# Optimization experiments

Hardware: AMD Instinct MI355X
Metric: run time of the kernel (lower is better)

## Reference

```python
import jax, jax.numpy as jnp
import numpy as np

BN_EPS = 1e-5

def lrelu(x):
    return jax.nn.leaky_relu(x, 0.2)

def bn(x, g, b):
    # BatchNorm1d in training mode: biased batch stats over batch dim
    m = x.mean(0)
    v = ((x - m) ** 2).mean(0)
    return g * (x - m) / jnp.sqrt(v + BN_EPS) + b

def setup_inputs() -> dict:
    key = jax.random.key(0)
    ks = jax.random.split(key, 12)
    B, NOISE, H, V = 128, 128, 512, 5000
    s = lambda *sh: 1.0 / np.sqrt(sh[-1])
    inp = {
        "z": jax.random.normal(ks[0], (B, NOISE), jnp.float32),
        "temperature": jnp.ones((1,), jnp.float32),
        "num_steps": 128,
        "W_z2h": jax.random.normal(ks[1], (H, NOISE), jnp.float32) * s(H, NOISE),
        "b_z2h": jnp.zeros((H,), jnp.float32),
        "g1": jnp.ones((H,), jnp.float32), "be1": jnp.zeros((H,), jnp.float32),
        "emb": jax.random.normal(ks[2], (V, H), jnp.float32),
        "g2": jnp.ones((2 * H,), jnp.float32), "be2": jnp.zeros((2 * H,), jnp.float32),
        "W_ih": jax.random.normal(ks[3], (3 * H, 2 * H), jnp.float32) * s(3 * H, 2 * H),
        "b_ih": jnp.zeros((3 * H,), jnp.float32),
        "W_hh": jax.random.normal(ks[4], (3 * H, H), jnp.float32) * s(3 * H, H),
        "b_hh": jnp.zeros((3 * H,), jnp.float32),
        "g3": jnp.ones((H,), jnp.float32), "be3": jnp.zeros((H,), jnp.float32),
        "W_h2o": jax.random.normal(ks[5], (V, H), jnp.float32) * s(V, H),
        "b_h2o": jnp.zeros((V,), jnp.float32),
    }
    return inp

def gru_cell(x, h, W_ih, b_ih, W_hh, b_hh):
    gi = x @ W_ih.T + b_ih
    gh = h @ W_hh.T + b_hh
    ir, iz, inn = jnp.split(gi, 3, axis=1)
    hr, hz, hn = jnp.split(gh, 3, axis=1)
    r = jax.nn.sigmoid(ir + hr)
    zt = jax.nn.sigmoid(iz + hz)
    n = jnp.tanh(inn + r * hn)
    return (1.0 - zt) * n + zt * h

def reference(z, temperature, W_z2h, b_z2h, g1, be1, emb, g2, be2,
              W_ih, b_ih, W_hh, b_hh, g3, be3, W_h2o, b_h2o, num_steps):
    V = W_h2o.shape[0]
    SOS = V - 1
    zbn = bn(lrelu(z @ W_z2h.T + b_z2h), g1, be1)  # [B,H]
    h0 = zbn
    prev0 = jnp.full((z.shape[0],), SOS, dtype=jnp.int32)
    key0 = jax.random.key(42)

    def step(carry, _):
        h, prev, key = carry
        key, sub = jax.random.split(key)
        x = lrelu(emb[prev])                                    # [B,H]
        si = bn(jnp.concatenate([x, zbn], axis=1), g2, be2)     # [B,2H]
        h = gru_cell(si, h, W_ih, b_ih, W_hh, b_hh)
        o = bn(lrelu(h), g3, be3)
        logits = o @ W_h2o.T + b_h2o                            # [B,V]
        u = jax.random.uniform(sub, logits.shape, jnp.float32, 1e-20, 1.0)
        gum = -jnp.log(-jnp.log(u))
        out = jax.nn.softmax((logits + gum) / temperature, axis=-1)
        prev = jnp.argmax(out, axis=-1).astype(jnp.int32)
        return (h, prev, key), out

    _, outs = jax.lax.scan(step, (h0, prev0, key0), None, length=num_steps)
    return jnp.transpose(outs, (1, 0, 2))  # [B, num_steps, V]
```

## Files before the change

### kernel.cpp

```cpp
#include <hip/hip_runtime.h>
#include <cstdint>
#include <cstddef>

#define B_SZ 128
#define NOISE_SZ 128
#define H 512
#define V_SZ 5000
#define BN_EPS 1e-5f

#define S1D 1099511627776.0
#define S2D 68719476736.0

#define SCRA_OFF 0
#define H_OFF    65536
#define GH_OFF   131072
#define GIZ_OFF  327680
#define SH_OFF   524288
#define SCRB_OFF 528896
#define AMX_OFF  594432

__device__ __forceinline__ uint32_t rotl32(uint32_t v, int r) {
  return (v << r) | (v >> (32 - r));
}

__device__ __forceinline__ void threefry2x32(uint32_t k0, uint32_t k1,
                                             uint32_t x0, uint32_t x1,
                                             uint32_t& o0, uint32_t& o1) {
  uint32_t k2 = k0 ^ k1 ^ 0x1BD11BDAu;
  x0 += k0; x1 += k1;
#define TFR(r) { x0 += x1; x1 = rotl32(x1, (r)); x1 ^= x0; }
  TFR(13) TFR(15) TFR(26) TFR(6)
  x0 += k1; x1 += k2 + 1u;
  TFR(17) TFR(29) TFR(16) TFR(24)
  x0 += k2; x1 += k0 + 2u;
  TFR(13) TFR(15) TFR(26) TFR(6)
  x0 += k0; x1 += k1 + 3u;
  TFR(17) TFR(29) TFR(16) TFR(24)
  x0 += k1; x1 += k2 + 4u;
  TFR(13) TFR(15) TFR(26) TFR(6)
  x0 += k2; x1 += k0 + 5u;
#undef TFR
  o0 = x0; o1 = x1;
}

struct U2 { uint32_t a, b; };
constexpr U2 tf_c(uint32_t k0, uint32_t k1, uint32_t x0, uint32_t x1) {
  uint32_t k2 = k0 ^ k1 ^ 0x1BD11BDAu;
  x0 += k0; x1 += k1;
#define TFRC(r) { x0 += x1; x1 = (uint32_t)((x1 << (r)) | (x1 >> (32 - (r)))); x1 ^= x0; }
  TFRC(13) TFRC(15) TFRC(26) TFRC(6)
  x0 += k1; x1 += k2 + 1u;
  TFRC(17) TFRC(29) TFRC(16) TFRC(24)
  x0 += k2; x1 += k0 + 2u;
  TFRC(13) TFRC(15) TFRC(26) TFRC(6)
  x0 += k0; x1 += k1 + 3u;
  TFRC(17) TFRC(29) TFRC(16) TFRC(24)
  x0 += k1; x1 += k2 + 4u;
  TFRC(13) TFRC(15) TFRC(26) TFRC(6)
  x0 += k2; x1 += k0 + 5u;
#undef TFRC
  return U2{x0, x1};
}

struct SubKeys { uint32_t v[512]; };
constexpr SubKeys make_subkeys() {
  SubKeys s{};
  uint32_t k0 = 0u, k1 = 42u;
  for (int t = 0; t < 256; ++t) {
    U2 nk = tf_c(k0, k1, 0u, 0u);
    U2 sb = tf_c(k0, k1, 0u, 1u);
    s.v[2 * t] = sb.a; s.v[2 * t + 1] = sb.b;
    k0 = nk.a; k1 = nk.b;
  }
  return s;
}
__device__ __constant__ SubKeys SUBK = make_subkeys();

__device__ __forceinline__ float lrelu_(float x) { return x >= 0.f ? x : 0.2f * x; }
__device__ __forceinline__ float sigmoidf_(float x) {
  return (x >= 0.f) ? 1.f / (1.f + expf(-x)) : expf(x) / (1.f + expf(x));
}

__device__ __forceinline__ void gemm32x64(
    const float* __restrict__ A, int lda,
    const float* __restrict__ W, int ldw, int K,
    int m0, int n0,
    const float* __restrict__ bias,
    bool relu,
    float* __restrict__ C, int ldc,
    float* smem) {
  float* As = smem;
  float* Ws = smem + 1216;
  const int tid = threadIdx.x;
  const int tn = tid & 15, tm = tid >> 4;
  const int amr = tid >> 3, aq = tid & 7;
  const int wnr = tid >> 2, wq = tid & 3;
  float acc[2][4] = {{0.f,0.f,0.f,0.f},{0.f,0.f,0.f,0.f}};
  for (int k0 = 0; k0 < K; k0 += 32) {
    const float4 av = *(const float4*)&A[(size_t)(m0 + amr) * lda + k0 + aq * 4];
    const float4 w0 = *(const float4*)&W[(size_t)(n0 + wnr) * ldw + k0 + wq * 4];
    const float4 w1 = *(const float4*)&W[(size_t)(n0 + wnr) * ldw + k0 + 16 + wq * 4];
    As[(aq * 4 + 0) * 38 + amr] = av.x;
    As[(aq * 4 + 1) * 38 + amr] = av.y;
    As[(aq * 4 + 2) * 38 + amr] = av.z;
    As[(aq * 4 + 3) * 38 + amr] = av.w;
    Ws[(wq * 4 + 0) * 68 + wnr] = w0.x;
    Ws[(wq * 4 + 1) * 68 + wnr] = w0.y;
    Ws[(wq * 4 + 2) * 68 + wnr] = w0.z;
    Ws[(wq * 4 + 3) * 68 + wnr] = w0.w;
    Ws[(16 + wq * 4 + 0) * 68 + wnr] = w1.x;
    Ws[(16 + wq * 4 + 1) * 68 + wnr] = w1.y;
    Ws[(16 + wq * 4 + 2) * 68 + wnr] = w1.z;
    Ws[(16 + wq * 4 + 3) * 68 + wnr] = w1.w;
    __syncthreads();
#pragma unroll
    for (int kk = 0; kk < 32; ++kk) {
      const float2 a2 = *(const float2*)&As[kk * 38 + tm * 2];
      const float4 b4 = *(const float4*)&Ws[kk * 68 + tn * 4];
      acc[0][0] = fmaf(a2.x, b4.x, acc[0][0]);
      acc[0][1] = fmaf(a2.x, b4.y, acc[0][1]);
      acc[0][2] = fmaf(a2.x, b4.z, acc[0][2]);
      acc[0][3] = fmaf(a2.x, b4.w, acc[0][3]);
      acc[1][0] = fmaf(a2.y, b4.x, acc[1][0]);
      acc[1][1] = fmaf(a2.y, b4.y, acc[1][1]);
      acc[1][2] = fmaf(a2.y, b4.z, acc[1][2]);
      acc[1][3] = fmaf(a2.y, b4.w, acc[1][3]);
    }
    __syncthreads();
  }
#pragma unroll
  for (int i = 0; i < 2; ++i) {
    const int m = m0 + tm * 2 + i;
#pragma unroll
    for (int j = 0; j < 4; ++j) {
      const int n = n0 + tn * 4 + j;
      float v = acc[i][j] + bias[n];
      if (relu) v = lrelu_(v);
      C[(size_t)m * ldc + n] = v;
    }
  }
}

__device__ __forceinline__ void bn8(const float* __restrict__ in,
                                    const float* __restrict__ g,
                                    const float* __restrict__ be,
                                    float* __restrict__ outp,
                                    float* __restrict__ out2, int c0) {
  const int col = c0 + (threadIdx.x >> 5);
  const int r = threadIdx.x & 31;
  float x0 = in[(size_t)r * H + col];
  float x1 = in[(size_t)(r + 32) * H + col];
  float x2 = in[(size_t)(r + 64) * H + col];
  float x3 = in[(size_t)(r + 96) * H + col];
  float s = x0 + x1 + x2 + x3;
#pragma unroll
  for (int m = 16; m; m >>= 1) s += __shfl_xor(s, m);
  const float mean = s * (1.f / 128.f);
  const float d0 = x0 - mean, d1 = x1 - mean, d2 = x2 - mean, d3 = x3 - mean;
  float q = d0 * d0 + d1 * d1 + d2 * d2 + d3 * d3;
#pragma unroll
  for (int m = 16; m; m >>= 1) q += __shfl_xor(q, m);
  const float v = q * (1.f / 128.f);
  const float sd = sqrtf(v + BN_EPS);
  const float gc = g[col], bc = be[col];
  const float y0 = gc * d0 / sd + bc;
  const float y1 = gc * d1 / sd + bc;
  const float y2 = gc * d2 / sd + bc;
  const float y3 = gc * d3 / sd + bc;
  outp[(size_t)r * H + col] = y0;
  outp[(size_t)(r + 32) * H + col] = y1;
  outp[(size_t)(r + 64) * H + col] = y2;
  outp[(size_t)(r + 96) * H + col] = y3;
  if (out2) {
    out2[(size_t)r * H + col] = y0;
    out2[(size_t)(r + 32) * H + col] = y1;
    out2[(size_t)(r + 64) * H + col] = y2;
    out2[(size_t)(r + 96) * H + col] = y3;
  }
}


__global__ __launch_bounds__(256, 2) void k_z2h(const float* __restrict__ z,
                                                const float* __restrict__ W,
                                                const float* __restrict__ bias,
                                                float* __restrict__ fws) {
  __shared__ float smem[3392];
  gemm32x64(z, NOISE_SZ, W, NOISE_SZ, NOISE_SZ,
            ((int)blockIdx.x & 3) * 32, ((int)blockIdx.x >> 2) * 64,
            bias, true, fws + SCRA_OFF, H, smem);
}

__global__ __launch_bounds__(256, 2) void k_bn1(const float* __restrict__ g1,
                                                const float* __restrict__ be1,
                                                float* __restrict__ fws) {
  bn8(fws + SCRA_OFF, g1, be1, fws + SCRB_OFF, fws + H_OFF, (int)blockIdx.x * 8);
}

__global__ __launch_bounds__(256, 2) void k_bn2(const float* __restrict__ g2,
                                                const float* __restrict__ be2,
                                                float* __restrict__ fws) {
  bn8(fws + SCRB_OFF, g2 + H, be2 + H, fws + SCRB_OFF, nullptr, (int)blockIdx.x * 8);
}

__global__ __launch_bounds__(256, 2) void k_setup4(
    const float* __restrict__ W_ih, const float* __restrict__ b_ih,
    const float* __restrict__ W_hh, const float* __restrict__ b_hh,
    float* __restrict__ fws) {
  __shared__ float smem[3392];
  const int blk = blockIdx.x;
  if (blk < 96) {
    gemm32x64(fws + SCRB_OFF, H, W_ih + H, 2 * H, H,
              (blk & 3) * 32, (blk >> 2) * 64,
              b_ih, false, fws + GIZ_OFF, 1536, smem);
  } else if (blk < 192) {
    const int b2 = blk - 96;
    gemm32x64(fws + H_OFF, H, W_hh, H, H,
              (b2 & 3) * 32, (b2 >> 2) * 64,
              b_hh, false, fws + GH_OFF, 1536, smem);
  } else {
    unsigned long long* sH = (unsigned long long*)(fws + SH_OFF);
    for (int i = threadIdx.x; i < 1024; i += 256) sH[i] = 0ull;
  }
}

__global__ __launch_bounds__(512, 2) void k_gates(
    const float* __restrict__ emb,
    const float* __restrict__ g2, const float* __restrict__ be2,
    const float* __restrict__ W_ih,
    float* __restrict__ fws, int t) {
  __shared__ float scs[512], shs[512];
  __shared__ int sidx[128];
  __shared__ float As[2 * 544];
  __shared__ float Ws[2 * 1664];
  __shared__ float sgi[2 * 800];
  const float* gi_z = fws + GIZ_OFF;
  const float* gh   = fws + GH_OFF;
  float* hbuf = fws + H_OFF;
  unsigned long long* statsH = (unsigned long long*)(fws + SH_OFF) + ((t & 1) ? 1024 : 0);
  unsigned long long* amax_prev = (unsigned long long*)(fws + AMX_OFF) + (((t + 1) & 1) ? 1024 : 0);
  unsigned long long* amax_cur  = (unsigned long long*)(fws + AMX_OFF) + ((t & 1) ? 1024 : 0);
  const int tid = threadIdx.x;
  const int kh = tid >> 8;
  const int tt = tid & 255;
  const int blk = blockIdx.x;
  const int m0 = (blk >> 5) * 16;
  const int c0 = (blk & 31) * 16;

  if (tid < 128) {
    sidx[tid] = (t == 0) ? (V_SZ - 1)
                         : (int)(~(uint32_t)(amax_prev[tid * 8] & 0xFFFFFFFFull));
    if (blk == 0) amax_cur[tid * 8] = 0ull;
  }
  __syncthreads();

  {
    double s = 0.0, q = 0.0;
    for (int b = 0; b < 128; ++b) {
      const float x = lrelu_(emb[(size_t)sidx[b] * H + tid]);
      s += x; q += (double)x * x;
    }
    const double md = s * (1.0 / 128.0);
    const double vd = q * (1.0 / 128.0) - md * md;
    const float sd = sqrtf((float)vd + BN_EPS);
    const float a = g2[tid] / sd;
    scs[tid] = a;
    shs[tid] = be2[tid] - (float)md * a;
  }
  __syncthreads();

  const int tm = tt >> 4, tn = tt & 15;
  const int amr = tt >> 3, aq = tt & 7;
  float* Ash = As + kh * 544;
  float* Wsh = Ws + kh * 1664;
  float acc0 = 0.f, acc1 = 0.f, acc2 = 0.f;
  for (int k0i = 0; k0i < 8; ++k0i) {
    const int k0 = kh * 256 + k0i * 32;
    if (tt < 128) {
      const float4 rv = *(const float4*)&emb[(size_t)sidx[m0 + amr] * H + k0 + aq * 4];
      const float4 a4 = *(const float4*)&scs[k0 + aq * 4];
      const float4 h4 = *(const float4*)&shs[k0 + aq * 4];
      float4 av;
      av.x = fmaf(lrelu_(rv.x), a4.x, h4.x);
      av.y = fmaf(lrelu_(rv.y), a4.y, h4.y);
      av.z = fmaf(lrelu_(rv.z), a4.z, h4.z);
      av.w = fmaf(lrelu_(rv.w), a4.w, h4.w);
      Ash[(aq * 4 + 0) * 17 + amr] = av.x;
      Ash[(aq * 4 + 1) * 17 + amr] = av.y;
      Ash[(aq * 4 + 2) * 17 + amr] = av.z;
      Ash[(aq * 4 + 3) * 17 + amr] = av.w;
    }
    {
      int i = tt;
#pragma unroll
      for (int rep = 0; rep < 2; ++rep) {
        if (i < 384) {
          const int wr = i >> 3, wq = i & 7;
          const int wrow = (wr < 16) ? (c0 + wr)
                         : (wr < 32) ? (512 + c0 + wr - 16)
                                     : (1024 + c0 + wr - 32);
          const float4 w = *(const float4*)&W_ih[(size_t)wrow * 1024 + k0 + wq * 4];
          Wsh[(wq * 4 + 0) * 52 + wr] = w.x;
          Wsh[(wq * 4 + 1) * 52 + wr] = w.y;
          Wsh[(wq * 4 + 2) * 52 + wr] = w.z;
          Wsh[(wq * 4 + 3) * 52 + wr] = w.w;
        }
        i += 256;
      }
    }
    __syncthreads();
#pragma unroll
    for (int kk = 0; kk < 32; ++kk) {
      const float a = Ash[kk * 17 + tm];
      acc0 = fmaf(a, Wsh[kk * 52 + tn], acc0);
      acc1 = fmaf(a, Wsh[kk * 52 + 16 + tn], acc1);
      acc2 = fmaf(a, Wsh[kk * 52 + 32 + tn], acc2);
    }
    __syncthreads();
  }
  sgi[kh * 800 + tm * 50 + tn]      = acc0;
  sgi[kh * 800 + tm * 50 + 16 + tn] = acc1;
  sgi[kh * 800 + tm * 50 + 32 + tn] = acc2;
  __syncthreads();

  long long* sred = (long long*)Ws;
  if (kh == 0) {
    const size_t gzb = (size_t)(m0 + tm) * 1536;
    const size_t ghb = gzb;
    const float gv0 = (sgi[tm * 50 + tn] + sgi[800 + tm * 50 + tn]) + gi_z[gzb + c0 + tn];
    const float gv1 = (sgi[tm * 50 + 16 + tn] + sgi[800 + tm * 50 + 16 + tn]) + gi_z[gzb + 512 + c0 + tn];
    const float gv2 = (sgi[tm * 50 + 32 + tn] + sgi[800 + tm * 50 + 32 + tn]) + gi_z[gzb + 1024 + c0 + tn];
    const float rr = sigmoidf_(gv0 + gh[ghb + c0 + tn]);
    const float zt = sigmoidf_(gv1 + gh[ghb + 512 + c0 + tn]);
    const float nn = tanhf(gv2 + rr * gh[ghb + 1024 + c0 + tn]);
    const size_t hix = (size_t)(m0 + tm) * H + c0 + tn;
    const float hold = hbuf[hix];
    const float hnew = (1.f - zt) * nn + zt * hold;
    hbuf[hix] = hnew;
    const float lx = lrelu_(hnew);
    sred[tt] = __double2ll_rn((double)lx * S1D);
    sred[256 + tt] = __double2ll_rn((double)lx * (double)lx * S2D);
  }
  __syncthreads();
  if (tid < 32) {
    const int c = tid & 15;
    long long s = 0;
    if (tid < 16) {
      for (int b = 0; b < 16; ++b) s += sred[c + 16 * b];
      atomicAdd(&statsH[c0 + c], (unsigned long long)s);
    } else {
      for (int b = 0; b < 16; ++b) s += sred[256 + c + 16 * b];
      atomicAdd(&statsH[512 + c0 + c], (unsigned long long)s);
    }
  }
}

__global__ __launch_bounds__(256, 3) void k_logits_gh(
    const float* __restrict__ W_h2o, const float* __restrict__ b_h2o,
    const float* __restrict__ W_hh, const float* __restrict__ b_hh,
    const float* __restrict__ g3, const float* __restrict__ be3,
    const float* __restrict__ temp_ptr, float* __restrict__ out,
    float* __restrict__ fws, int t, int T) {
  __shared__ float smem[4928];
  const int blk = blockIdx.x;
  const int tid = threadIdx.x;
  unsigned long long* statsAll = (unsigned long long*)(fws + SH_OFF);
  if (blk < 96) {
    if (blk == 0) {
      unsigned long long* othr = statsAll + (((t + 1) & 1) ? 1024 : 0);
      for (int i = tid; i < 1024; i += 256) othr[i] = 0ull;
    }
    gemm32x64(fws + H_OFF, H, W_hh, H, H,
              (blk & 3) * 32, (blk >> 2) * 64,
              b_hh, false, fws + GH_OFF, 1536, smem);
    return;
  }
  const int blk2 = blk - 96;
  float* As = smem;
  float* Ws2 = smem + 544;
  float* scs = smem + 3232;
  float* shs = smem + 3744;
  const unsigned long long* sH = statsAll + ((t & 1) ? 1024 : 0);
  for (int c = tid; c < 512; c += 256) {
    const double sm = (double)(long long)sH[c] * (1.0 / (128.0 * S1D));
    const double e2 = (double)(long long)sH[512 + c] * (1.0 / (128.0 * S2D));
    const double var = e2 - sm * sm;
    const float sd = sqrtf((float)var + BN_EPS);
    const float a = g3[c] / sd;
    scs[c] = a; shs[c] = be3[c] - (float)sm * a;
  }
  __syncthreads();

  const float* hbuf = fws + H_OFF;
  const int m0 = (blk2 & 7) * 16, n0 = (blk2 >> 3) * 80;
  const int tm = tid >> 4, tn = tid & 15;
  const int amr = tid >> 3, aq = tid & 7;
  float acc[5] = {0.f, 0.f, 0.f, 0.f, 0.f};
  for (int k0 = 0; k0 < 512; k0 += 32) {
    if (tid < 128) {
      const float4 hv = *(const float4*)&hbuf[(size_t)(m0 + amr) * 512 + k0 + aq * 4];
      const float4 a4 = *(const float4*)&scs[k0 + aq * 4];
      const float4 c4 = *(const float4*)&shs[k0 + aq * 4];
      float4 av;
      av.x = fmaf(lrelu_(hv.x), a4.x, c4.x);
      av.y = fmaf(lrelu_(hv.y), a4.y, c4.y);
      av.z = fmaf(lrelu_(hv.z), a4.z, c4.z);
      av.w = fmaf(lrelu_(hv.w), a4.w, c4.w);
      As[(aq * 4 + 0) * 17 + amr] = av.x;
      As[(aq * 4 + 1) * 17 + amr] = av.y;
      As[(aq * 4 + 2) * 17 + amr] = av.z;
      As[(aq * 4 + 3) * 17 + amr] = av.w;
    }
    for (int i = tid; i < 640; i += 256) {
      const int row = i >> 3, q = i & 7;
      float4 w = {0.f, 0.f, 0.f, 0.f};
      if (n0 + row < V_SZ)
        w = *(const float4*)&W_h2o[(size_t)(n0 + row) * 512 + k0 + q * 4];
      Ws2[(q * 4 + 0) * 84 + row] = w.x;
      Ws2[(q * 4 + 1) * 84 + row] = w.y;
      Ws2[(q * 4 + 2) * 84 + row] = w.z;
      Ws2[(q * 4 + 3) * 84 + row] = w.w;
    }
    __syncthreads();
#pragma unroll
    for (int kk = 0; kk < 32; ++kk) {
      const float a = As[kk * 17 + tm];
      const float4 b4 = *(const float4*)&Ws2[kk * 84 + tn * 4];
      const float b1 = Ws2[kk * 84 + 64 + tn];
      acc[0] = fmaf(a, b4.x, acc[0]);
      acc[1] = fmaf(a, b4.y, acc[1]);
      acc[2] = fmaf(a, b4.z, acc[2]);
      acc[3] = fmaf(a, b4.w, acc[3]);
      acc[4] = fmaf(a, b1,   acc[4]);
    }
    __syncthreads();
  }
  const float temp = temp_ptr[0];
  const uint32_t sk0 = SUBK.v[2 * t], sk1 = SUBK.v[2 * t + 1];
  const int m = m0 + tm;
  float* rowp = out + ((size_t)m * T + t) * V_SZ;
  unsigned long long bkey = 0ull;
#pragma unroll
  for (int j = 0; j < 5; ++j) {
    const int n = (j < 4) ? (n0 + tn * 4 + j) : (n0 + 64 + tn);
    if (n < V_SZ) {
      const float logit = acc[j] + b_h2o[n];
      uint32_t r0, r1;
      threefry2x32(sk0, sk1, 0u, (uint32_t)(m * V_SZ + n), r0, r1);
      const uint32_t bits = r0 ^ r1;
      const float f = __uint_as_float((bits >> 9) | 0x3f800000u) - 1.0f;
      const float u = fmaxf(1e-20f, f + 1e-20f);
      const float gum = -logf(-logf(u));
      const float y = (logit + gum) / temp;
      rowp[n] = y;
      uint32_t ub = __float_as_uint(y);
      ub = (ub & 0x80000000u) ? ~ub : (ub | 0x80000000u);
      const unsigned long long key =
          ((unsigned long long)ub << 32) | (unsigned long long)(~(uint32_t)n);
      if (key > bkey) bkey = key;
    }
  }
#pragma unroll
  for (int mk = 1; mk < 16; mk <<= 1) {
    const unsigned long long o = __shfl_xor(bkey, mk);
    if (o > bkey) bkey = o;
  }
  if (tn == 0) {
    unsigned long long* am = (unsigned long long*)(fws + AMX_OFF) + ((t & 1) ? 1024 : 0);
    atomicMax(&am[m * 8], bkey);
  }
}

__global__ __launch_bounds__(256, 2) void k_soft(float* __restrict__ out, int T) {
  __shared__ float sy[V_SZ];
  __shared__ float red[256];
  const int bid = blockIdx.x;
  const int b = bid / T, t = bid - b * T;
  const int tid = threadIdx.x;
  float* row = out + ((size_t)b * T + t) * V_SZ;

  float lmax = -3.4e38f;
  for (int j = tid; j < V_SZ; j += 256) {
    const float y = row[j];
    sy[j] = y;
    lmax = fmaxf(lmax, y);
  }
  red[tid] = lmax; __syncthreads();
#pragma unroll
  for (int s = 128; s > 0; s >>= 1) {
    if (tid < s) red[tid] = fmaxf(red[tid], red[tid + s]);
    __syncthreads();
  }
  const float m = red[0];
  __syncthreads();

  float lsum = 0.f;
  for (int j = tid; j < V_SZ; j += 256) {
    const float e = expf(sy[j] - m); sy[j] = e; lsum += e;
  }
  red[tid] = lsum; __syncthreads();
#pragma unroll
  for (int s = 128; s > 0; s >>= 1) {
    if (tid < s) red[tid] += red[tid + s];
    __syncthreads();
  }
  const float S = red[0];
  __syncthreads();

  for (int j = tid; j < V_SZ; j += 256) row[j] = sy[j] / S;
}

extern "C" void kernel_launch(void* const* d_in, const int* in_sizes, int n_in,
                              void* d_out, int out_size, void* d_ws, size_t ws_size,
                              hipStream_t stream) {
  const float* z     = (const float*)d_in[0];
  const float* temp  = (const float*)d_in[1];
  const float* W_z2h = (const float*)d_in[3];
  const float* b_z2h = (const float*)d_in[4];
  const float* g1    = (const float*)d_in[5];
  const float* be1   = (const float*)d_in[6];
  const float* emb   = (const float*)d_in[7];
  const float* g2    = (const float*)d_in[8];
  const float* be2   = (const float*)d_in[9];
  const float* W_ih  = (const float*)d_in[10];
  const float* b_ih  = (const float*)d_in[11];
  const float* W_hh  = (const float*)d_in[12];
  const float* b_hh  = (const float*)d_in[13];
  const float* g3    = (const float*)d_in[14];
  const float* be3   = (const float*)d_in[15];
  const float* W_h2o = (const float*)d_in[16];
  const float* b_h2o = (const float*)d_in[17];
  float* out = (float*)d_out;
  float* fws = (float*)d_ws;
  const int T = out_size / (B_SZ * V_SZ);

  k_z2h<<<32, 256, 0, stream>>>(z, W_z2h, b_z2h, fws);
  k_bn1<<<64, 256, 0, stream>>>(g1, be1, fws);
  k_bn2<<<64, 256, 0, stream>>>(g2, be2, fws);
  k_setup4<<<193, 256, 0, stream>>>(W_ih, b_ih, W_hh, b_hh, fws);

  for (int t = 0; t < T; ++t) {
    k_gates<<<256, 512, 0, stream>>>(emb, g2, be2, W_ih, fws, t);
    k_logits_gh<<<600, 256, 0, stream>>>(W_h2o, b_h2o, W_hh, b_hh, g3, be3,
                                         temp, out, fws, t, T);
  }

  k_soft<<<B_SZ * T, 256, 0, stream>>>(out, T);
}
```

Baseline: 9.952 ms.

## Use 4x4 register tiles with 128-thread blocks in the fused logits/gh kernel

The fused per-step kernel moves from 256-thread blocks with 1x5 or 2x4 outputs per thread to 128-thread blocks that each compute a 32x64 tile, with every thread holding a 4x4 register block fed by float4 shared-memory reads. The grid shrinks from 600 to 412 blocks, and logits are written with vectorized float4 stores. The goal is more FMAs per shared-memory load and fewer redundant W_h2o tile loads. In exchange there are fewer threads per block, more registers per thread, and 412 blocks may leave some compute units lightly loaded.

```diff
diff --git a/kernel.cpp b/kernel.cpp
--- a/kernel.cpp
+++ b/kernel.cpp
@@ -141,6 +141,75 @@
   }
 }
 
+__device__ __forceinline__ void gemm32x64_r44(
+    const float* __restrict__ A, int lda,
+    const float* __restrict__ W, int ldw, int K,
+    int m0, int n0,
+    const float* __restrict__ bias,
+    float* __restrict__ C, int ldc,
+    float* smem) {
+  float* As = smem;
+  float* Ws = smem + 1152;
+  const int tid = threadIdx.x;
+  const int tx = tid & 15, ty = tid >> 4;
+  float acc[4][4] = {{0,0,0,0},{0,0,0,0},{0,0,0,0},{0,0,0,0}};
+  for (int k0 = 0; k0 < K; k0 += 32) {
+#pragma unroll
+    for (int u = 0; u < 2; ++u) {
+      const int uu = tid + u * 128;
+      const int m = uu >> 3, q = uu & 7;
+      const float4 a = *(const float4*)&A[(size_t)(m0 + m) * lda + k0 + q * 4];
+      As[(q * 4 + 0) * 36 + m] = a.x;
+      As[(q * 4 + 1) * 36 + m] = a.y;
+      As[(q * 4 + 2) * 36 + m] = a.z;
+      As[(q * 4 + 3) * 36 + m] = a.w;
+    }
+#pragma unroll
+    for (int u = 0; u < 4; ++u) {
+      const int uu = tid + u * 128;
+      const int n = uu >> 3, q = uu & 7;
+      const float4 w = *(const float4*)&W[(size_t)(n0 + n) * ldw + k0 + q * 4];
+      Ws[(q * 4 + 0) * 68 + n] = w.x;
+      Ws[(q * 4 + 1) * 68 + n] = w.y;
+      Ws[(q * 4 + 2) * 68 + n] = w.z;
+      Ws[(q * 4 + 3) * 68 + n] = w.w;
+    }
+    __syncthreads();
+#pragma unroll
+    for (int kk = 0; kk < 32; ++kk) {
+      const float4 a4 = *(const float4*)&As[kk * 36 + ty * 4];
+      const float4 w4 = *(const float4*)&Ws[kk * 68 + tx * 4];
+      acc[0][0] = fmaf(a4.x, w4.x, acc[0][0]);
+      acc[0][1] = fmaf(a4.x, w4.y, acc[0][1]);
+      acc[0][2] = fmaf(a4.x, w4.z, acc[0][2]);
+      acc[0][3] = fmaf(a4.x, w4.w, acc[0][3]);
+      acc[1][0] = fmaf(a4.y, w4.x, acc[1][0]);
+      acc[1][1] = fmaf(a4.y, w4.y, acc[1][1]);
+      acc[1][2] = fmaf(a4.y, w4.z, acc[1][2]);
+      acc[1][3] = fmaf(a4.y, w4.w, acc[1][3]);
+      acc[2][0] = fmaf(a4.z, w4.x, acc[2][0]);
+      acc[2][1] = fmaf(a4.z, w4.y, acc[2][1]);
+      acc[2][2] = fmaf(a4.z, w4.z, acc[2][2]);
+      acc[2][3] = fmaf(a4.z, w4.w, acc[2][3]);
+      acc[3][0] = fmaf(a4.w, w4.x, acc[3][0]);
+      acc[3][1] = fmaf(a4.w, w4.y, acc[3][1]);
+      acc[3][2] = fmaf(a4.w, w4.z, acc[3][2]);
+      acc[3][3] = fmaf(a4.w, w4.w, acc[3][3]);
+    }
+    __syncthreads();
+  }
+#pragma unroll
+  for (int i = 0; i < 4; ++i) {
+    const int m = m0 + ty * 4 + i;
+    float4 v;
+    v.x = acc[i][0] + bias[n0 + tx * 4 + 0];
+    v.y = acc[i][1] + bias[n0 + tx * 4 + 1];
+    v.z = acc[i][2] + bias[n0 + tx * 4 + 2];
+    v.w = acc[i][3] + bias[n0 + tx * 4 + 3];
+    *(float4*)&C[(size_t)m * ldc + n0 + tx * 4] = v;
+  }
+}
+
 __device__ __forceinline__ void bn8(const float* __restrict__ in,
                                     const float* __restrict__ g,
                                     const float* __restrict__ be,
@@ -354,33 +423,33 @@
   }
 }
 
-__global__ __launch_bounds__(256, 3) void k_logits_gh(
+__global__ __launch_bounds__(128, 2) void k_logits_gh(
     const float* __restrict__ W_h2o, const float* __restrict__ b_h2o,
     const float* __restrict__ W_hh, const float* __restrict__ b_hh,
     const float* __restrict__ g3, const float* __restrict__ be3,
     const float* __restrict__ temp_ptr, float* __restrict__ out,
     float* __restrict__ fws, int t, int T) {
-  __shared__ float smem[4928];
+  __shared__ float smem[4352];
   const int blk = blockIdx.x;
   const int tid = threadIdx.x;
   unsigned long long* statsAll = (unsigned long long*)(fws + SH_OFF);
   if (blk < 96) {
     if (blk == 0) {
       unsigned long long* othr = statsAll + (((t + 1) & 1) ? 1024 : 0);
-      for (int i = tid; i < 1024; i += 256) othr[i] = 0ull;
-    }
-    gemm32x64(fws + H_OFF, H, W_hh, H, H,
-              (blk & 3) * 32, (blk >> 2) * 64,
-              b_hh, false, fws + GH_OFF, 1536, smem);
+      for (int i = tid; i < 1024; i += 128) othr[i] = 0ull;
+    }
+    gemm32x64_r44(fws + H_OFF, H, W_hh, H, H,
+                  (blk & 3) * 32, (blk >> 2) * 64,
+                  b_hh, fws + GH_OFF, 1536, smem);
     return;
   }
   const int blk2 = blk - 96;
   float* As = smem;
-  float* Ws2 = smem + 544;
-  float* scs = smem + 3232;
-  float* shs = smem + 3744;
+  float* Ws = smem + 1152;
+  float* scs = smem + 3328;
+  float* shs = smem + 3840;
   const unsigned long long* sH = statsAll + ((t & 1) ? 1024 : 0);
-  for (int c = tid; c < 512; c += 256) {
+  for (int c = tid; c < 512; c += 128) {
     const double sm = (double)(long long)sH[c] * (1.0 / (128.0 * S1D));
     const double e2 = (double)(long long)sH[512 + c] * (1.0 / (128.0 * S2D));
     const double var = e2 - sm * sm;
@@ -391,82 +460,112 @@
   __syncthreads();
 
   const float* hbuf = fws + H_OFF;
-  const int m0 = (blk2 & 7) * 16, n0 = (blk2 >> 3) * 80;
-  const int tm = tid >> 4, tn = tid & 15;
-  const int amr = tid >> 3, aq = tid & 7;
-  float acc[5] = {0.f, 0.f, 0.f, 0.f, 0.f};
+  const int m0 = (blk2 & 3) * 32, n0 = (blk2 >> 2) * 64;
+  const int tx = tid & 15, ty = tid >> 4;
+  float acc[4][4] = {{0,0,0,0},{0,0,0,0},{0,0,0,0},{0,0,0,0}};
   for (int k0 = 0; k0 < 512; k0 += 32) {
-    if (tid < 128) {
-      const float4 hv = *(const float4*)&hbuf[(size_t)(m0 + amr) * 512 + k0 + aq * 4];
-      const float4 a4 = *(const float4*)&scs[k0 + aq * 4];
-      const float4 c4 = *(const float4*)&shs[k0 + aq * 4];
-      float4 av;
-      av.x = fmaf(lrelu_(hv.x), a4.x, c4.x);
-      av.y = fmaf(lrelu_(hv.y), a4.y, c4.y);
-      av.z = fmaf(lrelu_(hv.z), a4.z, c4.z);
-      av.w = fmaf(lrelu_(hv.w), a4.w, c4.w);
-      As[(aq * 4 + 0) * 17 + amr] = av.x;
-      As[(aq * 4 + 1) * 17 + amr] = av.y;
-      As[(aq * 4 + 2) * 17 + amr] = av.z;
-      As[(aq * 4 + 3) * 17 + amr] = av.w;
-    }
-    for (int i = tid; i < 640; i += 256) {
-      const int row = i >> 3, q = i & 7;
+#pragma unroll
+    for (int u = 0; u < 2; ++u) {
+      const int uu = tid + u * 128;
+      const int m = uu >> 3, q = uu & 7;
+      const float4 hv = *(const float4*)&hbuf[(size_t)(m0 + m) * 512 + k0 + q * 4];
+      const float4 a4 = *(const float4*)&scs[k0 + q * 4];
+      const float4 c4 = *(const float4*)&shs[k0 + q * 4];
+      As[(q * 4 + 0) * 36 + m] = fmaf(lrelu_(hv.x), a4.x, c4.x);
+      As[(q * 4 + 1) * 36 + m] = fmaf(lrelu_(hv.y), a4.y, c4.y);
+      As[(q * 4 + 2) * 36 + m] = fmaf(lrelu_(hv.z), a4.z, c4.z);
+      As[(q * 4 + 3) * 36 + m] = fmaf(lrelu_(hv.w), a4.w, c4.w);
+    }
+#pragma unroll
+    for (int u = 0; u < 4; ++u) {
+      const int uu = tid + u * 128;
+      const int n = uu >> 3, q = uu & 7;
       float4 w = {0.f, 0.f, 0.f, 0.f};
-      if (n0 + row < V_SZ)
-        w = *(const float4*)&W_h2o[(size_t)(n0 + row) * 512 + k0 + q * 4];
-      Ws2[(q * 4 + 0) * 84 + row] = w.x;
-      Ws2[(q * 4 + 1) * 84 + row] = w.y;
-      Ws2[(q * 4 + 2) * 84 + row] = w.z;
-      Ws2[(q * 4 + 3) * 84 + row] = w.w;
+      if (n0 + n < V_SZ)
+        w = *(const float4*)&W_h2o[(size_t)(n0 + n) * 512 + k0 + q * 4];
+      Ws[(q * 4 + 0) * 68 + n] = w.x;
+      Ws[(q * 4 + 1) * 68 + n] = w.y;
+      Ws[(q * 4 + 2) * 68 + n] = w.z;
+      Ws[(q * 4 + 3) * 68 + n] = w.w;
     }
     __syncthreads();
 #pragma unroll
     for (int kk = 0; kk < 32; ++kk) {
-      const float a = As[kk * 17 + tm];
-      const float4 b4 = *(const float4*)&Ws2[kk * 84 + tn * 4];
-      const float b1 = Ws2[kk * 84 + 64 + tn];
-      acc[0] = fmaf(a, b4.x, acc[0]);
-      acc[1] = fmaf(a, b4.y, acc[1]);
-      acc[2] = fmaf(a, b4.z, acc[2]);
-      acc[3] = fmaf(a, b4.w, acc[3]);
-      acc[4] = fmaf(a, b1,   acc[4]);
-    }
-    __syncthreads();
-  }
+      const float4 a4 = *(const float4*)&As[kk * 36 + ty * 4];
+      const float4 w4 = *(const float4*)&Ws[kk * 68 + tx * 4];
+      acc[0][0] = fmaf(a4.x, w4.x, acc[0][0]);
+      acc[0][1] = fmaf(a4.x, w4.y, acc[0][1]);
+      acc[0][2] = fmaf(a4.x, w4.z, acc[0][2]);
+      acc[0][3] = fmaf(a4.x, w4.w, acc[0][3]);
+      acc[1][0] = fmaf(a4.y, w4.x, acc[1][0]);
+      acc[1][1] = fmaf(a4.y, w4.y, acc[1][1]);
+      acc[1][2] = fmaf(a4.y, w4.z, acc[1][2]);
+      acc[1][3] = fmaf(a4.y, w4.w, acc[1][3]);
+      acc[2][0] = fmaf(a4.z, w4.x, acc[2][0]);
+      acc[2][1] = fmaf(a4.z, w4.y, acc[2][1]);
+      acc[2][2] = fmaf(a4.z, w4.z, acc[2][2]);
+      acc[2][3] = fmaf(a4.z, w4.w, acc[2][3]);
+      acc[3][0] = fmaf(a4.w, w4.x, acc[3][0]);
+      acc[3][1] = fmaf(a4.w, w4.y, acc[3][1]);
+      acc[3][2] = fmaf(a4.w, w4.z, acc[3][2]);
+      acc[3][3] = fmaf(a4.w, w4.w, acc[3][3]);
+    }
+    __syncthreads();
+  }
+
   const float temp = temp_ptr[0];
   const uint32_t sk0 = SUBK.v[2 * t], sk1 = SUBK.v[2 * t + 1];
-  const int m = m0 + tm;
-  float* rowp = out + ((size_t)m * T + t) * V_SZ;
-  unsigned long long bkey = 0ull;
-#pragma unroll
-  for (int j = 0; j < 5; ++j) {
-    const int n = (j < 4) ? (n0 + tn * 4 + j) : (n0 + 64 + tn);
-    if (n < V_SZ) {
-      const float logit = acc[j] + b_h2o[n];
-      uint32_t r0, r1;
-      threefry2x32(sk0, sk1, 0u, (uint32_t)(m * V_SZ + n), r0, r1);
-      const uint32_t bits = r0 ^ r1;
-      const float f = __uint_as_float((bits >> 9) | 0x3f800000u) - 1.0f;
-      const float u = fmaxf(1e-20f, f + 1e-20f);
-      const float gum = -logf(-logf(u));
-      const float y = (logit + gum) / temp;
-      rowp[n] = y;
-      uint32_t ub = __float_as_uint(y);
-      ub = (ub & 0x80000000u) ? ~ub : (ub | 0x80000000u);
-      const unsigned long long key =
-          ((unsigned long long)ub << 32) | (unsigned long long)(~(uint32_t)n);
-      if (key > bkey) bkey = key;
+  const int nbase = n0 + tx * 4;
+  unsigned long long bkey[4] = {0ull, 0ull, 0ull, 0ull};
+#pragma unroll
+  for (int i = 0; i < 4; ++i) {
+    const int m = m0 + ty * 4 + i;
+    float* rowp = out + ((size_t)m * T + t) * V_SZ;
+    float yv[4];
+#pragma unroll
+    for (int j = 0; j < 4; ++j) {
+      const int n = nbase + j;
+      if (n < V_SZ) {
+        const float logit = acc[i][j] + b_h2o[n];
+        uint32_t r0, r1;
+        threefry2x32(sk0, sk1, 0u, (uint32_t)(m * V_SZ + n), r0, r1);
+        const uint32_t bits = r0 ^ r1;
+        const float f = __uint_as_float((bits >> 9) | 0x3f800000u) - 1.0f;
+        const float u = fmaxf(1e-20f, f + 1e-20f);
+        const float gum = -logf(-logf(u));
+        const float y = (logit + gum) / temp;
+        yv[j] = y;
+        uint32_t ub = __float_as_uint(y);
+        ub = (ub & 0x80000000u) ? ~ub : (ub | 0x80000000u);
+        const unsigned long long key =
+            ((unsigned long long)ub << 32) | (unsigned long long)(~(uint32_t)n);
+        if (key > bkey[i]) bkey[i] = key;
+      } else {
+        yv[j] = 0.f;
+      }
+    }
+    if (nbase + 3 < V_SZ) {
+      float4 v4; v4.x = yv[0]; v4.y = yv[1]; v4.z = yv[2]; v4.w = yv[3];
+      *(float4*)&rowp[nbase] = v4;
+    } else {
+#pragma unroll
+      for (int j = 0; j < 4; ++j)
+        if (nbase + j < V_SZ) rowp[nbase + j] = yv[j];
     }
   }
 #pragma unroll
   for (int mk = 1; mk < 16; mk <<= 1) {
-    const unsigned long long o = __shfl_xor(bkey, mk);
-    if (o > bkey) bkey = o;
-  }
-  if (tn == 0) {
+#pragma unroll
+    for (int i = 0; i < 4; ++i) {
+      const unsigned long long o = __shfl_xor(bkey[i], mk);
+      if (o > bkey[i]) bkey[i] = o;
+    }
+  }
+  if (tx == 0) {
     unsigned long long* am = (unsigned long long*)(fws + AMX_OFF) + ((t & 1) ? 1024 : 0);
-    atomicMax(&am[m * 8], bkey);
+#pragma unroll
+    for (int i = 0; i < 4; ++i)
+      atomicMax(&am[(m0 + ty * 4 + i) * 8], bkey[i]);
   }
 }
 
@@ -540,7 +639,7 @@
 
   for (int t = 0; t < T; ++t) {
     k_gates<<<256, 512, 0, stream>>>(emb, g2, be2, W_ih, fws, t);
-    k_logits_gh<<<600, 256, 0, stream>>>(W_h2o, b_h2o, W_hh, b_hh, g3, be3,
+    k_logits_gh<<<412, 128, 0, stream>>>(W_h2o, b_h2o, W_hh, b_hh, g3, be3,
                                          temp, out, fws, t, T);
   }
 
```

Measured after the change: 11.35 ms. 1.14x slower.
